# Kernel optimization log

Measured on AMD Instinct MI355X. Metric: run time of the kernel, lower is better.

## Reference

```python
import jax, jax.numpy as jnp
import numpy as np

GAMMA = 0.9865
B, S, D = 8, 2048, 128


def setup_inputs() -> dict:
    key = jax.random.key(0)
    kq, kk, kv, kw = jax.random.split(key, 4)
    xq = jax.random.normal(kq, (B, S, D), dtype=jnp.float32)
    xk = jax.random.normal(kk, (B, S, D), dtype=jnp.float32)
    xv = jax.random.normal(kv, (B, S, D), dtype=jnp.float32)
    # NOTE: the original builds three Dense layers by repeating the SAME object,
    # so Q/K/V share a single no-bias weight matrix W.
    W = jax.random.normal(kw, (D, D), dtype=jnp.float32) * (1.0 / np.sqrt(D))
    return {"xq": xq, "xk": xk, "xv": xv, "W": W}


def _decay_matrix(seq_len, gamma):
    # Original: factors[i,j] = gamma^(i-j); keep upper triangle (j>=i); transpose.
    # Result: Dm[n,m] = gamma^(m-n) for n >= m, else 0 (lower triangular).
    n = jnp.arange(seq_len, dtype=jnp.float32)
    expo = n[None, :] - n[:, None]            # [S,S], entry (n,m) = m - n
    Dm = jnp.tril(jnp.float32(gamma) ** expo)  # zero out m > n before they'd matter
    return Dm


def reference(xq, xk, xv, W):
    Q = xq @ W
    K = xk @ W
    V = xv @ W
    d = Q.shape[-1]
    scores = jnp.einsum('bnd,bmd->bnm', Q, K) / jnp.sqrt(jnp.float32(d))
    Dm = _decay_matrix(Q.shape[1], GAMMA)
    # D /= reduce_sum(D, axis=1) ** 0.5  -> row-sums broadcast over LAST axis,
    # i.e. column m of D is divided by sqrt(rowsum[m]). Faithful to tf broadcasting.
    Dm = Dm / jnp.sqrt(jnp.sum(Dm, axis=1))
    scores = scores * Dm
    # per-batch norm: xs[n,m] / max(|sum_k xs[m,k]|, 1)  (tf broadcasting over last axis)
    s = jnp.sum(scores, axis=2)                       # [B,S]
    scores = scores / jnp.maximum(jnp.abs(s), 1.0)[:, None, :]
    return scores @ V
```

## Files before the change

### kernel.cpp

```cpp
#include <hip/hip_runtime.h>
#include <math.h>


constexpr int B = 8, S = 2048, D = 128;
constexpr int C = 64, NC = S / C;
constexpr int BS = B * S;
constexpr int NCH = B * NC;
#define GAMMA_F 0.9865f

typedef __attribute__((ext_vector_type(8))) short short8;
typedef __attribute__((ext_vector_type(8))) unsigned short ushort8;
typedef __attribute__((ext_vector_type(4))) float f32x4;

__device__ inline unsigned short f2bf(float f) {
  unsigned u = __builtin_bit_cast(unsigned, f);
  return (unsigned short)((u + 0x7FFF + ((u >> 16) & 1)) >> 16);
}
__device__ inline float bf2f(unsigned short h) {
  return __builtin_bit_cast(float, (unsigned)h << 16);
}

__global__ void k_init(const float* __restrict__ W, unsigned short* __restrict__ wt,
                       float* __restrict__ qs, float* __restrict__ ks) {
  int bid = blockIdx.x, tid = threadIdx.x;
  if (bid < 64) {
    int idx = bid * 256 + tid;
    int k = idx & 127, c = idx >> 7;
    wt[c * 128 + k] = f2bf(W[k * 128 + c]);
  } else {
    int n = (bid - 64) * 256 + tid;
    if (n < S) {
      double g = (double)GAMMA_F;
      double lg = log(g);
      double gmn = exp(-lg * (double)n);
      double gn  = exp(lg * (double)n);
      double ginv = 1.0 / g;
      double rs = (exp(log(ginv) * (double)(n + 1)) - 1.0) / (ginv - 1.0);
      qs[n] = (float)(gmn / sqrt(128.0));
      ks[n] = (float)(gn / sqrt(rs));
    }
  }
}

__global__ __launch_bounds__(256) void k_proj(
    const float* __restrict__ xq, const float* __restrict__ xk,
    const float* __restrict__ xv, const unsigned short* __restrict__ wt,
    const float* __restrict__ qs, const float* __restrict__ ks,
    unsigned short* __restrict__ qb, unsigned short* __restrict__ kb,
    unsigned short* __restrict__ vb, float* __restrict__ cs) {
  __shared__ float css[4][128];
  int mat = blockIdx.y;
  const float* X = (mat == 0) ? xq : ((mat == 1) ? xk : xv);
  unsigned short* Ob = (mat == 0) ? qb : ((mat == 1) ? kb : vb);

  int tid = threadIdx.x, w = tid >> 6, lane = tid & 63;
  int bc = blockIdx.x;
  int r0 = bc * 64 + w * 16;
  int arow = r0 + (lane & 15);
  int kg = (lane >> 4) * 8;

  f32x4 acc[8];
#pragma unroll
  for (int j = 0; j < 8; j++) acc[j] = (f32x4){0.f, 0.f, 0.f, 0.f};
#pragma unroll
  for (int t = 0; t < 4; t++) {
    int k0 = t * 32 + kg;
    const float* ap = X + (size_t)arow * 128 + k0;
    float a8[8];
    *(f32x4*)(a8) = *(const f32x4*)ap;
    *(f32x4*)(a8 + 4) = *(const f32x4*)(ap + 4);
    short8 af;
#pragma unroll
    for (int i = 0; i < 8; i++) af[i] = (short)f2bf(a8[i]);
#pragma unroll
    for (int j = 0; j < 8; j++) {
      short8 bf = *(const short8*)(wt + (size_t)(j * 16 + (lane & 15)) * 128 + k0);
      acc[j] = __builtin_amdgcn_mfma_f32_16x16x32_bf16(af, bf, acc[j], 0, 0, 0);
    }
  }
  int crow = r0 + (lane >> 4) * 4;
  float csp[8];
#pragma unroll
  for (int j = 0; j < 8; j++) csp[j] = 0.f;
#pragma unroll
  for (int rr = 0; rr < 4; rr++) {
    int row = crow + rr;
    int n = row & (S - 1);
    float sc = (mat == 0) ? qs[n] : ((mat == 1) ? ks[n] : 1.0f);
#pragma unroll
    for (int j = 0; j < 8; j++) {
      float v = acc[j][rr] * sc;
      Ob[(size_t)row * 128 + j * 16 + (lane & 15)] = f2bf(v);
      csp[j] += v;
    }
  }
  if (mat == 1) {
#pragma unroll
    for (int j = 0; j < 8; j++) {
      csp[j] += __shfl_xor(csp[j], 16);
      csp[j] += __shfl_xor(csp[j], 32);
    }
    if ((lane >> 4) == 0)
#pragma unroll
      for (int j = 0; j < 8; j++) css[w][j * 16 + lane] = csp[j];
  }
  __syncthreads();
  if (mat == 1 && tid < 128)
    cs[bc * 128 + tid] = css[0][tid] + css[1][tid] + css[2][tid] + css[3][tid];
}

__global__ __launch_bounds__(512) void k_mid(
    const unsigned short* __restrict__ qb, const unsigned short* __restrict__ kb,
    const unsigned short* __restrict__ vb, const float* __restrict__ cs,
    unsigned short* __restrict__ al, unsigned short* __restrict__ vbT,
    unsigned short* __restrict__ Hc) {
  __shared__ unsigned short kraw[64][136];
  __shared__ unsigned short kT[128][72];
  __shared__ unsigned short vT[128][72];
  __shared__ float csp[128];
  __shared__ float invl[64];
  __shared__ float rsum_l[2][64];
  int bc = blockIdx.x, b = bc >> 5, c = bc & 31;
  int tid = threadIdx.x, w = tid >> 6, lane = tid & 63;
  int l15 = lane & 15;
  int kg = (lane >> 4) * 8;
  size_t base = (size_t)bc * C * D;

  if (tid < 128) {
    float a = 0.f;
    for (int cc = 0; cc < c; cc++) a += cs[(size_t)(b * NC + cc) * 128 + tid];
    csp[tid] = a;
  }

  {
    int rt = w & 3, mh = w >> 2;
    int arow = rt * 16 + l15;
    int crow = rt * 16 + (lane >> 4) * 4;
    f32x4 a1[2];
#pragma unroll
    for (int mi = 0; mi < 2; mi++) a1[mi] = (f32x4){0.f, 0.f, 0.f, 0.f};
#pragma unroll
    for (int t = 0; t < 4; t++) {
      int k0 = t * 32 + kg;
      short8 af = *(const short8*)(qb + base + (size_t)arow * D + k0);
#pragma unroll
      for (int mi = 0; mi < 2; mi++) {
        int mt = mh * 2 + mi;
        short8 bf = *(const short8*)(kb + base + (size_t)(mt * 16 + l15) * D + k0);
        a1[mi] = __builtin_amdgcn_mfma_f32_16x16x32_bf16(af, bf, a1[mi], 0, 0, 0);
      }
    }
    unsigned short* alg = al + (size_t)bc * 64 * 64;
    float rsp[4] = {0.f, 0.f, 0.f, 0.f};
#pragma unroll
    for (int mi = 0; mi < 2; mi++)
#pragma unroll
      for (int rr = 0; rr < 4; rr++) {
        int n_l = crow + rr, m_l = (mh * 2 + mi) * 16 + l15;
        float mv = (n_l >= m_l) ? a1[mi][rr] : 0.f;
        alg[n_l * 64 + m_l] = f2bf(mv);
        rsp[rr] += mv;
      }
#pragma unroll
    for (int rr = 0; rr < 4; rr++) {
      float r = rsp[rr];
      r += __shfl_xor(r, 1); r += __shfl_xor(r, 2);
      r += __shfl_xor(r, 4); r += __shfl_xor(r, 8);
      if (l15 == 0) rsum_l[mh][crow + rr] = r;
    }
  }
#pragma unroll
  for (int i = 0; i < 2; i++) {
    int e = (i * 512 + tid) * 8;
    *(ushort8*)&kraw[e >> 7][e & 127] = *(const ushort8*)(kb + base + e);
  }
  __syncthreads();

  {
    int row = tid >> 3, part = tid & 7;
    const unsigned short* q = qb + base + (size_t)row * D + part * 16;
    ushort8 q8a = *(const ushort8*)q;
    ushort8 q8b = *(const ushort8*)(q + 8);
    float dot = 0.f;
#pragma unroll
    for (int ii = 0; ii < 8; ii++) {
      dot = fmaf(bf2f(q8a[ii]), csp[part * 16 + ii], dot);
      dot = fmaf(bf2f(q8b[ii]), csp[part * 16 + 8 + ii], dot);
    }
    dot += __shfl_xor(dot, 1); dot += __shfl_xor(dot, 2); dot += __shfl_xor(dot, 4);
    if (part == 0) {
      float s = rsum_l[0][row] + rsum_l[1][row] + dot;
      invl[row] = 1.f / fmaxf(fabsf(s), 1.f);
    }
  }
  {
    int d = tid & 127, mh2 = tid >> 7;
#pragma unroll
    for (int mg = 0; mg < 2; mg++) {
      ushort8 pk;
#pragma unroll
      for (int i = 0; i < 8; i++) pk[i] = kraw[mh2 * 16 + mg * 8 + i][d];
      *(ushort8*)&kT[d][mh2 * 16 + mg * 8] = pk;
    }
  }
  __syncthreads();
#pragma unroll
  for (int i = 0; i < 2; i++) {
    int e = (i * 512 + tid) * 8;
    int row = e >> 7, col = e & 127;
    ushort8 v8 = *(const ushort8*)(vb + base + e);
    float inv = invl[row];
    ushort8 o;
#pragma unroll
    for (int ii = 0; ii < 8; ii++) o[ii] = f2bf(bf2f(v8[ii]) * inv);
    *(ushort8*)&kraw[row][col] = o;
  }
  __syncthreads();
  {
    int d = tid & 127, mh2 = tid >> 7;
#pragma unroll
    for (int mg = 0; mg < 2; mg++) {
      ushort8 pk;
#pragma unroll
      for (int i = 0; i < 8; i++) pk[i] = kraw[mh2 * 16 + mg * 8 + i][d];
      *(ushort8*)&vT[d][mh2 * 16 + mg * 8] = pk;
    }
  }
  __syncthreads();
  {
    f32x4 hacc[8];
#pragma unroll
    for (int j = 0; j < 8; j++) hacc[j] = (f32x4){0.f, 0.f, 0.f, 0.f};
#pragma unroll
    for (int t = 0; t < 2; t++) {
      int k0 = t * 32 + kg;
      short8 a2 = *(const short8*)&vT[w * 16 + l15][k0];
#pragma unroll
      for (int j = 0; j < 8; j++) {
        short8 bf = *(const short8*)&kT[j * 16 + l15][k0];
        hacc[j] = __builtin_amdgcn_mfma_f32_16x16x32_bf16(a2, bf, hacc[j], 0, 0, 0);
      }
    }
    unsigned short* g = Hc + (size_t)bc * D * D;
#pragma unroll
    for (int j = 0; j < 8; j++)
#pragma unroll
      for (int rr = 0; rr < 4; rr++)
        g[(size_t)(w * 16 + (lane >> 4) * 4 + rr) * D + j * 16 + l15] =
            f2bf(hacc[j][rr]);
  }
  {
    int d = tid >> 2, pp = (tid & 3) * 16;
    unsigned short* dst = vbT + (size_t)bc * D * C + (size_t)d * C + pp;
    *(ushort8*)(dst) = *(ushort8*)&vT[d][pp];
    *(ushort8*)(dst + 8) = *(ushort8*)&vT[d][pp + 8];
  }
}

__global__ __launch_bounds__(64) void k_gscan(const unsigned short* __restrict__ Hc,
                                              unsigned short* __restrict__ HS) {
  int b = blockIdx.x, gy = blockIdx.y, t = threadIdx.x;
  int d2 = gy * 4 + (t >> 4), d1 = (t & 15) * 8;
  size_t off = ((size_t)(b * NC) * D + d2) * D + d1;
  ushort8 v[NC];
#pragma unroll
  for (int c = 0; c < NC; c++)
    v[c] = *(const ushort8*)(Hc + off + (size_t)c * D * D);
  float run[8];
#pragma unroll
  for (int j = 0; j < 8; j++) run[j] = 0.f;
#pragma unroll
  for (int c = 0; c < NC; c++) {
    ushort8 o;
#pragma unroll
    for (int j = 0; j < 8; j++) {
      o[j] = f2bf(run[j]);
      run[j] += bf2f(v[c][j]);
    }
    *(ushort8*)(HS + off + (size_t)c * D * D) = o;
  }
}

__global__ __launch_bounds__(512) void k_out(
    const unsigned short* __restrict__ qb, const unsigned short* __restrict__ al,
    const unsigned short* __restrict__ vbT, const unsigned short* __restrict__ HS,
    float* __restrict__ out) {
  int bc = blockIdx.x, tid = threadIdx.x, w = tid >> 6, lane = tid & 63;
  int l15 = lane & 15;
  size_t base = (size_t)bc * C * D;
  int kg = (lane >> 4) * 8;
  int rt = w >> 1, ch = w & 1;
  int arow = rt * 16 + l15;
  int crow = rt * 16 + (lane >> 4) * 4;

  f32x4 acc[4];
#pragma unroll
  for (int j = 0; j < 4; j++) acc[j] = (f32x4){0.f, 0.f, 0.f, 0.f};
  const unsigned short* hrow = HS + (size_t)bc * D * D;
#pragma unroll
  for (int t = 0; t < 4; t++) {
    int k0 = t * 32 + kg;
    short8 af = *(const short8*)(qb + base + (size_t)arow * D + k0);
#pragma unroll
    for (int jj = 0; jj < 4; jj++) {
      int j = ch * 4 + jj;
      short8 bf = *(const short8*)(hrow + (size_t)(j * 16 + l15) * D + k0);
      acc[jj] = __builtin_amdgcn_mfma_f32_16x16x32_bf16(af, bf, acc[jj], 0, 0, 0);
    }
  }
  const unsigned short* alg = al + (size_t)bc * 64 * 64;
  const unsigned short* vt = vbT + (size_t)bc * D * C;
#pragma unroll
  for (int t = 0; t < 2; t++) {
    int k0 = t * 32 + kg;
    short8 af = *(const short8*)(alg + (size_t)arow * 64 + k0);
#pragma unroll
    for (int jj = 0; jj < 4; jj++) {
      int j = ch * 4 + jj;
      short8 bf = *(const short8*)(vt + (size_t)(j * 16 + l15) * C + k0);
      acc[jj] = __builtin_amdgcn_mfma_f32_16x16x32_bf16(af, bf, acc[jj], 0, 0, 0);
    }
  }
#pragma unroll
  for (int jj = 0; jj < 4; jj++)
#pragma unroll
    for (int rr = 0; rr < 4; rr++)
      out[base + (size_t)(crow + rr) * D + (ch * 4 + jj) * 16 + l15] = acc[jj][rr];
}

extern "C" void kernel_launch(void* const* d_in, const int* in_sizes, int n_in,
                              void* d_out, int out_size, void* d_ws, size_t ws_size,
                              hipStream_t stream) {
  const float* xq = (const float*)d_in[0];
  const float* xk = (const float*)d_in[1];
  const float* xv = (const float*)d_in[2];
  const float* W  = (const float*)d_in[3];
  float* out = (float*)d_out;

  char* p = (char*)d_ws;
  unsigned short* qb  = (unsigned short*)p;  p += (size_t)BS * D * 2;
  unsigned short* kb  = (unsigned short*)p;  p += (size_t)BS * D * 2;
  unsigned short* vb  = (unsigned short*)p;  p += (size_t)BS * D * 2;
  unsigned short* vbT = (unsigned short*)p;  p += (size_t)NCH * D * C * 2;
  unsigned short* al  = (unsigned short*)p;  p += (size_t)NCH * C * C * 2;
  unsigned short* Hc  = (unsigned short*)p;  p += (size_t)NCH * D * D * 2;
  unsigned short* HS  = (unsigned short*)p;  p += (size_t)NCH * D * D * 2;
  unsigned short* wt  = (unsigned short*)p;  p += (size_t)D * D * 2;
  float* cs = (float*)p;                     p += (size_t)NCH * D * 4;
  float* qs = (float*)p;                     p += (size_t)S * 4;
  float* ks = (float*)p;                     p += (size_t)S * 4;

  hipLaunchKernelGGL(k_init, dim3(72), dim3(256), 0, stream, W, wt, qs, ks);
  hipLaunchKernelGGL(k_proj, dim3(NCH, 3), dim3(256), 0, stream,
                     xq, xk, xv, wt, qs, ks, qb, kb, vb, cs);
  hipLaunchKernelGGL(k_mid, dim3(NCH), dim3(512), 0, stream, qb, kb, vb, cs,
                     al, vbT, Hc);
  hipLaunchKernelGGL(k_gscan, dim3(B, 32), dim3(64), 0, stream, Hc, HS);
  hipLaunchKernelGGL(k_out, dim3(NCH), dim3(512), 0, stream, qb, al, vbT, HS, out);
}
```

Measured before the change: 59.04 us.

## Fuse QKV projection into chunk kernel and precompute K column sums from raw input

Merges the init, projection and mid-stage kernels into one per-chunk kernel that converts W into LDS, projects Q/K/V into shared memory and consumes them directly, so K and V are never written to or reread from global memory. The decay-scaled K column sums are now computed before projection (a small kernel sums scaled raw xk rows, then the result is multiplied by W), and the scale factors are computed inline in float. This removes two launches and the global K/V round trip. In exchange each block transposes W again, uses more shared memory (likely lowering occupancy), and float exp replaces double-precision scale math.

```diff
diff --git a/kernel.cpp b/kernel.cpp
--- a/kernel.cpp
+++ b/kernel.cpp
@@ -20,133 +20,132 @@
   return __builtin_bit_cast(float, (unsigned)h << 16);
 }
 
-__global__ void k_init(const float* __restrict__ W, unsigned short* __restrict__ wt,
-                       float* __restrict__ qs, float* __restrict__ ks) {
-  int bid = blockIdx.x, tid = threadIdx.x;
-  if (bid < 64) {
-    int idx = bid * 256 + tid;
-    int k = idx & 127, c = idx >> 7;
-    wt[c * 128 + k] = f2bf(W[k * 128 + c]);
-  } else {
-    int n = (bid - 64) * 256 + tid;
-    if (n < S) {
-      double g = (double)GAMMA_F;
-      double lg = log(g);
-      double gmn = exp(-lg * (double)n);
-      double gn  = exp(lg * (double)n);
-      double ginv = 1.0 / g;
-      double rs = (exp(log(ginv) * (double)(n + 1)) - 1.0) / (ginv - 1.0);
-      qs[n] = (float)(gmn / sqrt(128.0));
-      ks[n] = (float)(gn / sqrt(rs));
-    }
-  }
-}
-
-__global__ __launch_bounds__(256) void k_proj(
+__global__ __launch_bounds__(128) void k_y(const float* __restrict__ xk,
+                                           float* __restrict__ yc) {
+  __shared__ float ksl[64];
+  int bc = blockIdx.x, tid = threadIdx.x;
+  float lgf = logf(GAMMA_F);
+  if (tid < 64) {
+    int n = (bc * 64 + tid) & (S - 1);
+    float rs = (expf(-lgf * (float)(n + 1)) - 1.f) * (GAMMA_F / (1.f - GAMMA_F));
+    ksl[tid] = expf(lgf * (float)n) / sqrtf(rs);
+  }
+  __syncthreads();
+  const float* x = xk + (size_t)bc * 64 * 128 + tid;
+  float a = 0.f;
+#pragma unroll
+  for (int j = 0; j < 64; j++) a = fmaf(ksl[j], x[j * 128], a);
+  yc[(size_t)bc * 128 + tid] = a;
+}
+
+__global__ __launch_bounds__(512) void k_big(
     const float* __restrict__ xq, const float* __restrict__ xk,
-    const float* __restrict__ xv, const unsigned short* __restrict__ wt,
-    const float* __restrict__ qs, const float* __restrict__ ks,
-    unsigned short* __restrict__ qb, unsigned short* __restrict__ kb,
-    unsigned short* __restrict__ vb, float* __restrict__ cs) {
-  __shared__ float css[4][128];
-  int mat = blockIdx.y;
-  const float* X = (mat == 0) ? xq : ((mat == 1) ? xk : xv);
-  unsigned short* Ob = (mat == 0) ? qb : ((mat == 1) ? kb : vb);
-
-  int tid = threadIdx.x, w = tid >> 6, lane = tid & 63;
-  int bc = blockIdx.x;
-  int r0 = bc * 64 + w * 16;
-  int arow = r0 + (lane & 15);
-  int kg = (lane >> 4) * 8;
-
-  f32x4 acc[8];
-#pragma unroll
-  for (int j = 0; j < 8; j++) acc[j] = (f32x4){0.f, 0.f, 0.f, 0.f};
-#pragma unroll
-  for (int t = 0; t < 4; t++) {
-    int k0 = t * 32 + kg;
-    const float* ap = X + (size_t)arow * 128 + k0;
-    float a8[8];
-    *(f32x4*)(a8) = *(const f32x4*)ap;
-    *(f32x4*)(a8 + 4) = *(const f32x4*)(ap + 4);
-    short8 af;
-#pragma unroll
-    for (int i = 0; i < 8; i++) af[i] = (short)f2bf(a8[i]);
-#pragma unroll
-    for (int j = 0; j < 8; j++) {
-      short8 bf = *(const short8*)(wt + (size_t)(j * 16 + (lane & 15)) * 128 + k0);
-      acc[j] = __builtin_amdgcn_mfma_f32_16x16x32_bf16(af, bf, acc[j], 0, 0, 0);
-    }
-  }
-  int crow = r0 + (lane >> 4) * 4;
-  float csp[8];
-#pragma unroll
-  for (int j = 0; j < 8; j++) csp[j] = 0.f;
-#pragma unroll
-  for (int rr = 0; rr < 4; rr++) {
-    int row = crow + rr;
-    int n = row & (S - 1);
-    float sc = (mat == 0) ? qs[n] : ((mat == 1) ? ks[n] : 1.0f);
-#pragma unroll
-    for (int j = 0; j < 8; j++) {
-      float v = acc[j][rr] * sc;
-      Ob[(size_t)row * 128 + j * 16 + (lane & 15)] = f2bf(v);
-      csp[j] += v;
-    }
-  }
-  if (mat == 1) {
-#pragma unroll
-    for (int j = 0; j < 8; j++) {
-      csp[j] += __shfl_xor(csp[j], 16);
-      csp[j] += __shfl_xor(csp[j], 32);
-    }
-    if ((lane >> 4) == 0)
-#pragma unroll
-      for (int j = 0; j < 8; j++) css[w][j * 16 + lane] = csp[j];
-  }
-  __syncthreads();
-  if (mat == 1 && tid < 128)
-    cs[bc * 128 + tid] = css[0][tid] + css[1][tid] + css[2][tid] + css[3][tid];
-}
-
-__global__ __launch_bounds__(512) void k_mid(
-    const unsigned short* __restrict__ qb, const unsigned short* __restrict__ kb,
-    const unsigned short* __restrict__ vb, const float* __restrict__ cs,
+    const float* __restrict__ xv, const float* __restrict__ W,
+    const float* __restrict__ yc, unsigned short* __restrict__ qb,
     unsigned short* __restrict__ al, unsigned short* __restrict__ vbT,
     unsigned short* __restrict__ Hc) {
-  __shared__ unsigned short kraw[64][136];
-  __shared__ unsigned short kT[128][72];
-  __shared__ unsigned short vT[128][72];
+  __shared__ unsigned short qkv[3][64][136];
+  __shared__ alignas(16) char ovl[36864];
   __shared__ float csp[128];
+  __shared__ float ysum[128];
+  __shared__ float cspp[4][128];
   __shared__ float invl[64];
   __shared__ float rsum_l[2][64];
+  auto wt = (unsigned short(*)[136])ovl;
+  auto kT = (unsigned short(*)[72])ovl;
+  auto vT = (unsigned short(*)[72])(ovl + 18432);
+
   int bc = blockIdx.x, b = bc >> 5, c = bc & 31;
   int tid = threadIdx.x, w = tid >> 6, lane = tid & 63;
-  int l15 = lane & 15;
-  int kg = (lane >> 4) * 8;
-  size_t base = (size_t)bc * C * D;
-
+  int l15 = lane & 15, kg = (lane >> 4) * 8;
+  float lgf = logf(GAMMA_F);
+
+  for (int idx = tid; idx < 128 * 128; idx += 512) {
+    int cc = idx >> 7, k = idx & 127;
+    wt[cc][k] = f2bf(W[k * 128 + cc]);
+  }
   if (tid < 128) {
     float a = 0.f;
-    for (int cc = 0; cc < c; cc++) a += cs[(size_t)(b * NC + cc) * 128 + tid];
-    csp[tid] = a;
-  }
-
-  {
-    int rt = w & 3, mh = w >> 2;
+    for (int cc = 0; cc < c; cc++) a += yc[(size_t)(b * NC + cc) * 128 + tid];
+    ysum[tid] = a;
+  }
+  __syncthreads();
+
+  int rt = w & 3, chh = w >> 2;
+  {
     int arow = rt * 16 + l15;
-    int crow = rt * 16 + (lane >> 4) * 4;
+    size_t grow = (size_t)(bc * 64 + arow) * 128;
+    for (int mat = 0; mat < 3; mat++) {
+      const float* X = (mat == 0) ? xq : ((mat == 1) ? xk : xv);
+      f32x4 acc[4];
+#pragma unroll
+      for (int j = 0; j < 4; j++) acc[j] = (f32x4){0.f, 0.f, 0.f, 0.f};
+#pragma unroll
+      for (int t = 0; t < 4; t++) {
+        int k0 = t * 32 + kg;
+        const float* ap = X + grow + k0;
+        float a8[8];
+        *(f32x4*)(a8) = *(const f32x4*)ap;
+        *(f32x4*)(a8 + 4) = *(const f32x4*)(ap + 4);
+        short8 af;
+#pragma unroll
+        for (int i = 0; i < 8; i++) af[i] = (short)f2bf(a8[i]);
+#pragma unroll
+        for (int j = 0; j < 4; j++) {
+          short8 bf = *(const short8*)&wt[(chh * 4 + j) * 16 + l15][k0];
+          acc[j] = __builtin_amdgcn_mfma_f32_16x16x32_bf16(af, bf, acc[j], 0, 0, 0);
+        }
+      }
+      int crow = rt * 16 + (lane >> 4) * 4;
+#pragma unroll
+      for (int rr = 0; rr < 4; rr++) {
+        int row = crow + rr;
+        int n = (bc * 64 + row) & (S - 1);
+        float sc;
+        if (mat == 0) {
+          sc = expf(-lgf * (float)n) * 0.088388347f;
+        } else if (mat == 1) {
+          float rs = (expf(-lgf * (float)(n + 1)) - 1.f) * (GAMMA_F / (1.f - GAMMA_F));
+          sc = expf(lgf * (float)n) / sqrtf(rs);
+        } else {
+          sc = 1.f;
+        }
+#pragma unroll
+        for (int j = 0; j < 4; j++)
+          qkv[mat][row][(chh * 4 + j) * 16 + l15] = f2bf(acc[j][rr] * sc);
+      }
+    }
+  }
+  {
+    int d = tid & 127, q = tid >> 7;
+    float part = 0.f;
+#pragma unroll
+    for (int k = 0; k < 32; k++) part = fmaf(ysum[32 * q + k], bf2f(wt[d][32 * q + k]), part);
+    cspp[q][d] = part;
+  }
+  __syncthreads();
+
+  if (tid < 128) csp[tid] = cspp[0][tid] + cspp[1][tid] + cspp[2][tid] + cspp[3][tid];
+  {
+    int row = tid >> 3, col = (tid & 7) * 16;
+    unsigned short* dst = qb + (size_t)(bc * 64 + row) * 128 + col;
+    *(ushort8*)dst = *(const ushort8*)&qkv[0][row][col];
+    *(ushort8*)(dst + 8) = *(const ushort8*)&qkv[0][row][col + 8];
+  }
+  {
+    int rt2 = w & 3, mh = w >> 2;
+    int arow = rt2 * 16 + l15;
+    int crow = rt2 * 16 + (lane >> 4) * 4;
     f32x4 a1[2];
 #pragma unroll
     for (int mi = 0; mi < 2; mi++) a1[mi] = (f32x4){0.f, 0.f, 0.f, 0.f};
 #pragma unroll
     for (int t = 0; t < 4; t++) {
       int k0 = t * 32 + kg;
-      short8 af = *(const short8*)(qb + base + (size_t)arow * D + k0);
+      short8 af = *(const short8*)&qkv[0][arow][k0];
 #pragma unroll
       for (int mi = 0; mi < 2; mi++) {
-        int mt = mh * 2 + mi;
-        short8 bf = *(const short8*)(kb + base + (size_t)(mt * 16 + l15) * D + k0);
+        short8 bf = *(const short8*)&qkv[1][(mh * 2 + mi) * 16 + l15][k0];
         a1[mi] = __builtin_amdgcn_mfma_f32_16x16x32_bf16(af, bf, a1[mi], 0, 0, 0);
       }
     }
@@ -169,18 +168,32 @@
       if (l15 == 0) rsum_l[mh][crow + rr] = r;
     }
   }
-#pragma unroll
-  for (int i = 0; i < 2; i++) {
-    int e = (i * 512 + tid) * 8;
-    *(ushort8*)&kraw[e >> 7][e & 127] = *(const ushort8*)(kb + base + e);
+  {
+    int d = tid & 127, mh2 = tid >> 7;
+#pragma unroll
+    for (int mg = 0; mg < 2; mg++) {
+      ushort8 pk;
+#pragma unroll
+      for (int i = 0; i < 8; i++) pk[i] = qkv[1][mh2 * 16 + mg * 8 + i][d];
+      *(ushort8*)&kT[d][mh2 * 16 + mg * 8] = pk;
+    }
+  }
+  {
+    int d = tid & 127, mh2 = tid >> 7;
+#pragma unroll
+    for (int mg = 0; mg < 2; mg++) {
+      ushort8 pk;
+#pragma unroll
+      for (int i = 0; i < 8; i++) pk[i] = qkv[2][mh2 * 16 + mg * 8 + i][d];
+      *(ushort8*)&vT[d][mh2 * 16 + mg * 8] = pk;
+    }
   }
   __syncthreads();
 
   {
     int row = tid >> 3, part = tid & 7;
-    const unsigned short* q = qb + base + (size_t)row * D + part * 16;
-    ushort8 q8a = *(const ushort8*)q;
-    ushort8 q8b = *(const ushort8*)(q + 8);
+    ushort8 q8a = *(const ushort8*)&qkv[0][row][part * 16];
+    ushort8 q8b = *(const ushort8*)&qkv[0][row][part * 16 + 8];
     float dot = 0.f;
 #pragma unroll
     for (int ii = 0; ii < 8; ii++) {
@@ -193,40 +206,21 @@
       invl[row] = 1.f / fmaxf(fabsf(s), 1.f);
     }
   }
-  {
-    int d = tid & 127, mh2 = tid >> 7;
-#pragma unroll
-    for (int mg = 0; mg < 2; mg++) {
-      ushort8 pk;
-#pragma unroll
-      for (int i = 0; i < 8; i++) pk[i] = kraw[mh2 * 16 + mg * 8 + i][d];
-      *(ushort8*)&kT[d][mh2 * 16 + mg * 8] = pk;
-    }
-  }
-  __syncthreads();
-#pragma unroll
-  for (int i = 0; i < 2; i++) {
-    int e = (i * 512 + tid) * 8;
-    int row = e >> 7, col = e & 127;
-    ushort8 v8 = *(const ushort8*)(vb + base + e);
-    float inv = invl[row];
-    ushort8 o;
-#pragma unroll
-    for (int ii = 0; ii < 8; ii++) o[ii] = f2bf(bf2f(v8[ii]) * inv);
-    *(ushort8*)&kraw[row][col] = o;
-  }
-  __syncthreads();
-  {
-    int d = tid & 127, mh2 = tid >> 7;
-#pragma unroll
-    for (int mg = 0; mg < 2; mg++) {
-      ushort8 pk;
-#pragma unroll
-      for (int i = 0; i < 8; i++) pk[i] = kraw[mh2 * 16 + mg * 8 + i][d];
-      *(ushort8*)&vT[d][mh2 * 16 + mg * 8] = pk;
-    }
-  }
-  __syncthreads();
+  __syncthreads();
+
+  {
+    int d = tid >> 2, ms = (tid & 3) * 16;
+#pragma unroll
+    for (int g = 0; g < 2; g++) {
+      ushort8 v8 = *(const ushort8*)&vT[d][ms + g * 8];
+      ushort8 o;
+#pragma unroll
+      for (int ii = 0; ii < 8; ii++) o[ii] = f2bf(bf2f(v8[ii]) * invl[ms + g * 8 + ii]);
+      *(ushort8*)&vT[d][ms + g * 8] = o;
+    }
+  }
+  __syncthreads();
+
   {
     f32x4 hacc[8];
 #pragma unroll
@@ -252,8 +246,8 @@
   {
     int d = tid >> 2, pp = (tid & 3) * 16;
     unsigned short* dst = vbT + (size_t)bc * D * C + (size_t)d * C + pp;
-    *(ushort8*)(dst) = *(ushort8*)&vT[d][pp];
-    *(ushort8*)(dst + 8) = *(ushort8*)&vT[d][pp + 8];
+    *(ushort8*)(dst) = *(const ushort8*)&vT[d][pp];
+    *(ushort8*)(dst + 8) = *(const ushort8*)&vT[d][pp + 8];
   }
 }
 
@@ -338,23 +332,16 @@
   float* out = (float*)d_out;
 
   char* p = (char*)d_ws;
+  float* yc = (float*)p;                     p += (size_t)NCH * D * 4;
   unsigned short* qb  = (unsigned short*)p;  p += (size_t)BS * D * 2;
-  unsigned short* kb  = (unsigned short*)p;  p += (size_t)BS * D * 2;
-  unsigned short* vb  = (unsigned short*)p;  p += (size_t)BS * D * 2;
+  unsigned short* al  = (unsigned short*)p;  p += (size_t)NCH * C * C * 2;
   unsigned short* vbT = (unsigned short*)p;  p += (size_t)NCH * D * C * 2;
-  unsigned short* al  = (unsigned short*)p;  p += (size_t)NCH * C * C * 2;
   unsigned short* Hc  = (unsigned short*)p;  p += (size_t)NCH * D * D * 2;
   unsigned short* HS  = (unsigned short*)p;  p += (size_t)NCH * D * D * 2;
-  unsigned short* wt  = (unsigned short*)p;  p += (size_t)D * D * 2;
-  float* cs = (float*)p;                     p += (size_t)NCH * D * 4;
-  float* qs = (float*)p;                     p += (size_t)S * 4;
-  float* ks = (float*)p;                     p += (size_t)S * 4;
-
-  hipLaunchKernelGGL(k_init, dim3(72), dim3(256), 0, stream, W, wt, qs, ks);
-  hipLaunchKernelGGL(k_proj, dim3(NCH, 3), dim3(256), 0, stream,
-                     xq, xk, xv, wt, qs, ks, qb, kb, vb, cs);
-  hipLaunchKernelGGL(k_mid, dim3(NCH), dim3(512), 0, stream, qb, kb, vb, cs,
-                     al, vbT, Hc);
+
+  hipLaunchKernelGGL(k_y, dim3(NCH), dim3(128), 0, stream, xk, yc);
+  hipLaunchKernelGGL(k_big, dim3(NCH), dim3(512), 0, stream,
+                     xq, xk, xv, W, yc, qb, al, vbT, Hc);
   hipLaunchKernelGGL(k_gscan, dim3(B, 32), dim3(64), 0, stream, Hc, HS);
   hipLaunchKernelGGL(k_out, dim3(NCH), dim3(512), 0, stream, qb, al, vbT, HS, out);
 }
```

Measured after the change: 51.78 us, median of 2. 1.14x faster.
